# Optimization experiments

Measured on AMD Instinct MI355X. Metric: run time of the kernel, lower is better.

## Reference

```python
import jax, jax.numpy as jnp
import numpy as np

N_QUBITS = 4
DIM = 2 ** N_QUBITS  # 16-dim statevector
KERNEL = 3
STRIDE = 1
PADDING = 1


def _rot_mats(w):
    # PennyLane Rot(phi, theta, omega) = RZ(omega) RY(theta) RZ(phi)
    phi, theta, omega = w[:, 0], w[:, 1], w[:, 2]
    c = jnp.cos(theta / 2)
    s = jnp.sin(theta / 2)
    em = jnp.exp(-0.5j * (phi + omega))
    ep = jnp.exp(0.5j * (phi + omega))
    ed = jnp.exp(0.5j * (phi - omega))
    edm = jnp.exp(-0.5j * (phi - omega))
    row0 = jnp.stack([em * c, -ed * s], axis=-1)
    row1 = jnp.stack([edm * s, ep * c], axis=-1)
    return jnp.stack([row0, row1], axis=-2)  # [n_qubits, 2, 2]


def _apply_1q(state, U, wire):
    # state: [M] + [2]*n, wire axis is 1+wire (wire 0 is most significant)
    s = jnp.moveaxis(state, 1 + wire, -1)
    s = jnp.einsum('...b,ab->...a', s, U)
    return jnp.moveaxis(s, -1, 1 + wire)


def _apply_cnot(state, c, t):
    s = jnp.moveaxis(state, (1 + c, 1 + t), (-2, -1))
    shp = s.shape
    s = s.reshape(shp[:-2] + (4,))[..., jnp.array([0, 1, 3, 2])].reshape(shp)
    return jnp.moveaxis(s, (-2, -1), (1 + c, 1 + t))


def _forward(x, W_pre, b_pre, W_post, b_post, q_weights):
    B, C, L = x.shape
    xp = jnp.pad(x, ((0, 0), (0, 0), (PADDING, PADDING)))
    L_out = (L + 2 * PADDING - KERNEL) // STRIDE + 1
    starts = jnp.arange(L_out) * STRIDE
    # windows: [B, C, L_out, K] -> flatten channel-major like torch reshape
    win = xp[:, :, starts[:, None] + jnp.arange(KERNEL)[None, :]]
    win = win.transpose(0, 2, 1, 3).reshape(B, L_out, C * KERNEL)
    pre = win @ W_pre.T + b_pre  # [B, L_out, n_qubits]
    # AmplitudeEmbedding: pad to 2**n and normalize
    v = jnp.pad(pre, ((0, 0), (0, 0), (0, DIM - N_QUBITS)))
    v = v / jnp.linalg.norm(v, axis=-1, keepdims=True)
    state = v.reshape(B * L_out, *([2] * N_QUBITS)).astype(jnp.complex64)
    U = _rot_mats(q_weights)
    for i in range(N_QUBITS):
        state = _apply_1q(state, U[i], i)
    for i in range(N_QUBITS - 1):
        state = _apply_cnot(state, i, i + 1)
    flat = state.reshape(B * L_out, DIM)
    probs = jnp.real(flat) ** 2 + jnp.imag(flat) ** 2
    # PauliZ expectation per wire: sign of bit i (wire 0 = MSB)
    bits = (jnp.arange(DIM)[None, :] >> (N_QUBITS - 1 - jnp.arange(N_QUBITS)[:, None])) & 1
    z = (1 - 2 * bits).astype(probs.dtype)  # [n_qubits, DIM]
    expz = (probs @ z.T).reshape(B, L_out, N_QUBITS)
    out = expz @ W_post.T + b_post  # [B, L_out, out_channels]
    return out.transpose(0, 2, 1)


def setup_inputs() -> dict:
    key = jax.random.key(0)
    ks = jax.random.split(key, 6)
    B, C, L = 32, 80, 3000
    OUT = 512
    return {
        'x': jax.random.normal(ks[0], (B, C, L), dtype=jnp.float32),
        'W_pre': jax.random.normal(ks[1], (N_QUBITS, C * KERNEL), dtype=jnp.float32) * 0.06,
        'b_pre': jax.random.normal(ks[2], (N_QUBITS,), dtype=jnp.float32) * 0.06,
        'W_post': jax.random.normal(ks[3], (OUT, N_QUBITS), dtype=jnp.float32) * 0.4,
        'b_post': jax.random.normal(ks[4], (OUT,), dtype=jnp.float32) * 0.4,
        'q_weights': jax.random.normal(ks[5], (N_QUBITS, 3), dtype=jnp.float32),
    }


def reference(x, W_pre, b_pre, W_post, b_post, q_weights):
    return _forward(x, W_pre, b_pre, W_post, b_post, q_weights)
```

## Files before the change

kernel.cpp:

```cpp
#include <hip/hip_runtime.h>
#include <math.h>

#define C_IN 80
#define L_IN 3000
#define OUT_C 512
#define NT 512
#define TL 128
#define CPT 20

struct c2f { float x, y; };

__device__ __forceinline__ c2f cmul(c2f a, c2f b) {
    return { a.x*b.x - a.y*b.y, a.x*b.y + a.y*b.x };
}
__device__ __forceinline__ c2f csel(c2f a, c2f b, int bit) {
    c2f r; r.x = bit ? b.x : a.x; r.y = bit ? b.y : a.y; return r;
}
__device__ __forceinline__ float quadform(const float4* __restrict__ A, float4 p) {
    float4 r0 = A[0], r1 = A[1], r2 = A[2], r3 = A[3];
    return p.x*(r0.x*p.x + r0.y*p.y + r0.z*p.z + r0.w*p.w)
         + p.y*(r1.x*p.x + r1.y*p.y + r1.z*p.z + r1.w*p.w)
         + p.z*(r2.x*p.x + r2.y*p.y + r2.z*p.z + r2.w*p.w)
         + p.w*(r3.x*p.x + r3.y*p.y + r3.z*p.z + r3.w*p.w);
}

__global__ __launch_bounds__(NT) void qconv_kernel(
    const float* __restrict__ x,
    const float* __restrict__ W_pre,
    const float* __restrict__ b_pre,
    const float* __restrict__ W_post,
    const float* __restrict__ b_post,
    const float* __restrict__ qw,
    float* __restrict__ out)
{
    __shared__ float4 s_wpre[C_IN*3];
    __shared__ float4 s_post[OUT_C];
    __shared__ float  s_bpost[OUT_C];
    __shared__ float4 s_A[4][4];
    __shared__ float4 s_part[3][TL];
    __shared__ float4 s_e[TL];

    const int t  = threadIdx.x;
    const int b  = blockIdx.y;
    const int l0 = blockIdx.x * TL;

    for (int i = t; i < C_IN*3; i += NT) {
        s_wpre[i] = make_float4(W_pre[0*C_IN*3 + i], W_pre[1*C_IN*3 + i],
                                W_pre[2*C_IN*3 + i], W_pre[3*C_IN*3 + i]);
    }
    if (t < OUT_C) {
        s_post[t]  = *reinterpret_cast<const float4*>(&W_post[t*4]);
        s_bpost[t] = b_post[t];
    }
    __syncthreads();

    if (t < 64) {
        c2f U[4][2][2];
        #pragma unroll
        for (int i = 0; i < 4; ++i) {
            float phi = qw[i*3+0], theta = qw[i*3+1], omega = qw[i*3+2];
            float sh, ch;  sincosf(0.5f*theta, &sh, &ch);
            float s1, c1;  sincosf(0.5f*(phi+omega), &s1, &c1);
            float s2, cv;  sincosf(0.5f*(phi-omega), &s2, &cv);
            U[i][0][0] = {  c1*ch, -s1*ch };
            U[i][0][1] = { -cv*sh, -s2*sh };
            U[i][1][0] = {  cv*sh, -s2*sh };
            U[i][1][1] = {  c1*ch,  s1*ch };
        }
        const int q  = t >> 4;
        const int j  = (t >> 2) & 3;
        const int jp = t & 3;
        const int j2  = (j  >> 1) & 1, j3  = j  & 1;
        const int jp2 = (jp >> 1) & 1, jp3 = jp & 1;
        float s = 0.f;
        #pragma unroll
        for (int k = 0; k < 16; ++k) {
            int m = k ^ ((k >> 1) & 1);
            m ^= ((m >> 2) & 1) << 1;
            m ^= ((m >> 3) & 1) << 2;
            const int m0 = (m >> 3) & 1, m1 = (m >> 2) & 1;
            const int m2 = (m >> 1) & 1, m3 = m & 1;
            c2f w01 = cmul(U[0][m0][0], U[1][m1][0]);
            c2f av = cmul(w01, cmul(csel(U[2][m2][0], U[2][m2][1], j2),
                                    csel(U[3][m3][0], U[3][m3][1], j3)));
            c2f bv = cmul(w01, cmul(csel(U[2][m2][0], U[2][m2][1], jp2),
                                    csel(U[3][m3][0], U[3][m3][1], jp3)));
            float z = 1.f - 2.f * ((k >> (3 - q)) & 1);
            s += z * (av.x*bv.x + av.y*bv.y);
        }
        ((float*)s_A)[t] = s;
    }

    const int i = t & (TL - 1);
    const int h = t >> 7;
    const int l = l0 + i;
    const bool lvalid = (l < L_IN);

    float4 acc = (h == 0) ? make_float4(b_pre[0], b_pre[1], b_pre[2], b_pre[3])
                          : make_float4(0.f, 0.f, 0.f, 0.f);
    if (lvalid) {
        const float* __restrict__ xrow = x + (size_t)b * C_IN * L_IN + (size_t)(h*CPT) * L_IN + l;
        const bool has_m1 = (l >= 1);
        const bool has_p1 = (l + 1 < L_IN);
        #pragma unroll 4
        for (int c = 0; c < CPT; ++c) {
            const float* r = xrow + c * L_IN;
            float xa = has_m1 ? r[-1] : 0.f;
            float xb = r[0];
            float xc = has_p1 ? r[1] : 0.f;
            const int ck = (h*CPT + c) * 3;
            float4 w0 = s_wpre[ck], w1 = s_wpre[ck+1], w2 = s_wpre[ck+2];
            acc.x += w0.x*xa + w1.x*xb + w2.x*xc;
            acc.y += w0.y*xa + w1.y*xb + w2.y*xc;
            acc.z += w0.z*xa + w1.z*xb + w2.z*xc;
            acc.w += w0.w*xa + w1.w*xb + w2.w*xc;
        }
    }
    if (h > 0) s_part[h-1][i] = acc;
    __syncthreads();

    if (t < TL && lvalid) {
        float4 p = acc;
        float4 p1 = s_part[0][t], p2 = s_part[1][t], p3 = s_part[2][t];
        p.x += p1.x + p2.x + p3.x;
        p.y += p1.y + p2.y + p3.y;
        p.z += p1.z + p2.z + p3.z;
        p.w += p1.w + p2.w + p3.w;
        const float inv = 1.f / (p.x*p.x + p.y*p.y + p.z*p.z + p.w*p.w);
        float4 e;
        e.x = quadform(s_A[0], p) * inv;
        e.y = quadform(s_A[1], p) * inv;
        e.z = quadform(s_A[2], p) * inv;
        e.w = quadform(s_A[3], p) * inv;
        s_e[t] = e;
    }
    __syncthreads();

    {
        const int lane = t & 63;
        const int w    = t >> 6;
        const int lc   = l0 + 2*lane;
        const bool v2  = (lc < L_IN);
        const float4 e0 = s_e[2*lane];
        const float4 e1 = s_e[2*lane + 1];
        float* op = out + (size_t)b * OUT_C * L_IN + (size_t)w * L_IN + lc;
        #pragma unroll 8
        for (int k = 0; k < OUT_C/8; ++k) {
            const int o = w + 8*k;
            float4 wv = s_post[o];
            float bb  = s_bpost[o];
            float2 st;
            st.x = wv.x*e0.x + wv.y*e0.y + wv.z*e0.z + wv.w*e0.w + bb;
            st.y = wv.x*e1.x + wv.y*e1.y + wv.z*e1.z + wv.w*e1.w + bb;
            if (v2) *reinterpret_cast<float2*>(op) = st;
            op += (size_t)8 * L_IN;
        }
    }
}

extern "C" void kernel_launch(void* const* d_in, const int* in_sizes, int n_in,
                              void* d_out, int out_size, void* d_ws, size_t ws_size,
                              hipStream_t stream) {
    const float* x      = (const float*)d_in[0];
    const float* W_pre  = (const float*)d_in[1];
    const float* b_pre  = (const float*)d_in[2];
    const float* W_post = (const float*)d_in[3];
    const float* b_post = (const float*)d_in[4];
    const float* qw     = (const float*)d_in[5];
    float* out = (float*)d_out;

    const int B = in_sizes[0] / (C_IN * L_IN);
    dim3 grid((L_IN + TL - 1) / TL, B);
    qconv_kernel<<<grid, NT, 0, stream>>>(x, W_pre, b_pre, W_post, b_post, qw, out);
}
```

Measured before the change: 43.81 us.

## Warp-specialize block so half computes second tile while other half stores first

The block's 128 positions are split into two halves. All 8 warps first compute the pre-projection for the first half, then warps 0-3 emit output rows for it while warps 4-7 compute the second half's projection. Afterwards every warp writes its own 64 output channels for both halves using scalar stores, replacing the earlier float2 stores. The aim is to overlap the input-read and reduction phase with the large output-write phase. It depends on __syncthreads being reached in divergent branches, which is fragile, and the scalar stores may be less efficient than the old float2 ones.

```diff
diff --git a/kernel.cpp b/kernel.cpp
--- a/kernel.cpp
+++ b/kernel.cpp
@@ -6,7 +6,6 @@
 #define OUT_C 512
 #define NT 512
 #define TL 128
-#define CPT 20
 
 struct c2f { float x, y; };
 
@@ -15,13 +14,6 @@
 }
 __device__ __forceinline__ c2f csel(c2f a, c2f b, int bit) {
     c2f r; r.x = bit ? b.x : a.x; r.y = bit ? b.y : a.y; return r;
-}
-__device__ __forceinline__ float quadform(const float4* __restrict__ A, float4 p) {
-    float4 r0 = A[0], r1 = A[1], r2 = A[2], r3 = A[3];
-    return p.x*(r0.x*p.x + r0.y*p.y + r0.z*p.z + r0.w*p.w)
-         + p.y*(r1.x*p.x + r1.y*p.y + r1.z*p.z + r1.w*p.w)
-         + p.z*(r2.x*p.x + r2.y*p.y + r2.z*p.z + r2.w*p.w)
-         + p.w*(r3.x*p.x + r3.y*p.y + r3.z*p.z + r3.w*p.w);
 }
 
 __global__ __launch_bounds__(NT) void qconv_kernel(
@@ -36,23 +28,22 @@
     __shared__ float4 s_wpre[C_IN*3];
     __shared__ float4 s_post[OUT_C];
     __shared__ float  s_bpost[OUT_C];
-    __shared__ float4 s_A[4][4];
-    __shared__ float4 s_part[3][TL];
-    __shared__ float4 s_e[TL];
-
-    const int t  = threadIdx.x;
-    const int b  = blockIdx.y;
-    const int l0 = blockIdx.x * TL;
+    __shared__ float4 s_A[16];
+    __shared__ float4 s_pA[8*64];
+    __shared__ float4 s_pB[4*64];
+
+    const int t    = threadIdx.x;
+    const int w    = t >> 6;
+    const int lane = t & 63;
+    const int b    = blockIdx.y;
+    const int l0   = blockIdx.x * TL;
 
     for (int i = t; i < C_IN*3; i += NT) {
         s_wpre[i] = make_float4(W_pre[0*C_IN*3 + i], W_pre[1*C_IN*3 + i],
                                 W_pre[2*C_IN*3 + i], W_pre[3*C_IN*3 + i]);
     }
-    if (t < OUT_C) {
-        s_post[t]  = *reinterpret_cast<const float4*>(&W_post[t*4]);
-        s_bpost[t] = b_post[t];
-    }
-    __syncthreads();
+    s_post[t]  = *reinterpret_cast<const float4*>(&W_post[t*4]);
+    s_bpost[t] = b_post[t];
 
     if (t < 64) {
         c2f U[4][2][2];
@@ -91,70 +82,130 @@
         ((float*)s_A)[t] = s;
     }
 
-    const int i = t & (TL - 1);
-    const int h = t >> 7;
-    const int l = l0 + i;
-    const bool lvalid = (l < L_IN);
-
-    float4 acc = (h == 0) ? make_float4(b_pre[0], b_pre[1], b_pre[2], b_pre[3])
-                          : make_float4(0.f, 0.f, 0.f, 0.f);
-    if (lvalid) {
-        const float* __restrict__ xrow = x + (size_t)b * C_IN * L_IN + (size_t)(h*CPT) * L_IN + l;
-        const bool has_m1 = (l >= 1);
-        const bool has_p1 = (l + 1 < L_IN);
-        #pragma unroll 4
-        for (int c = 0; c < CPT; ++c) {
-            const float* r = xrow + c * L_IN;
-            float xa = has_m1 ? r[-1] : 0.f;
-            float xb = r[0];
-            float xc = has_p1 ? r[1] : 0.f;
-            const int ck = (h*CPT + c) * 3;
-            float4 w0 = s_wpre[ck], w1 = s_wpre[ck+1], w2 = s_wpre[ck+2];
-            acc.x += w0.x*xa + w1.x*xb + w2.x*xc;
-            acc.y += w0.y*xa + w1.y*xb + w2.y*xc;
-            acc.z += w0.z*xa + w1.z*xb + w2.z*xc;
-            acc.w += w0.w*xa + w1.w*xb + w2.w*xc;
-        }
-    }
-    if (h > 0) s_part[h-1][i] = acc;
+    {
+        const int l = l0 + lane;
+        const bool lv = (l < L_IN);
+        float4 acc = (w == 0) ? make_float4(b_pre[0], b_pre[1], b_pre[2], b_pre[3])
+                              : make_float4(0.f, 0.f, 0.f, 0.f);
+        if (lv) {
+            const float* __restrict__ xr = x + (size_t)b * C_IN * L_IN + (size_t)(w*10) * L_IN + l;
+            const bool hm = (l >= 1), hp = (l + 1 < L_IN);
+            #pragma unroll
+            for (int c = 0; c < 10; ++c) {
+                const float* r = xr + c * L_IN;
+                float xa = hm ? r[-1] : 0.f;
+                float xb = r[0];
+                float xc = hp ? r[1] : 0.f;
+                const int ck = (w*10 + c) * 3;
+                float4 w0 = s_wpre[ck], w1 = s_wpre[ck+1], w2 = s_wpre[ck+2];
+                acc.x += w0.x*xa + w1.x*xb + w2.x*xc;
+                acc.y += w0.y*xa + w1.y*xb + w2.y*xc;
+                acc.z += w0.z*xa + w1.z*xb + w2.z*xc;
+                acc.w += w0.w*xa + w1.w*xb + w2.w*xc;
+            }
+        }
+        s_pA[w*64 + lane] = acc;
+    }
     __syncthreads();
 
-    if (t < TL && lvalid) {
-        float4 p = acc;
-        float4 p1 = s_part[0][t], p2 = s_part[1][t], p3 = s_part[2][t];
-        p.x += p1.x + p2.x + p3.x;
-        p.y += p1.y + p2.y + p3.y;
-        p.z += p1.z + p2.z + p3.z;
-        p.w += p1.w + p2.w + p3.w;
+    auto reduceA = [&]() {
+        float4 p = s_pA[lane];
+        #pragma unroll
+        for (int j = 1; j < 8; ++j) {
+            float4 q2 = s_pA[j*64 + lane];
+            p.x += q2.x; p.y += q2.y; p.z += q2.z; p.w += q2.w;
+        }
+        return p;
+    };
+    auto reduceB = [&]() {
+        float4 p = s_pB[lane];
+        #pragma unroll
+        for (int j = 1; j < 4; ++j) {
+            float4 q2 = s_pB[j*64 + lane];
+            p.x += q2.x; p.y += q2.y; p.z += q2.z; p.w += q2.w;
+        }
+        return p;
+    };
+    auto expz = [&](float4 p) {
         const float inv = 1.f / (p.x*p.x + p.y*p.y + p.z*p.z + p.w*p.w);
         float4 e;
-        e.x = quadform(s_A[0], p) * inv;
-        e.y = quadform(s_A[1], p) * inv;
-        e.z = quadform(s_A[2], p) * inv;
-        e.w = quadform(s_A[3], p) * inv;
-        s_e[t] = e;
-    }
-    __syncthreads();
-
-    {
-        const int lane = t & 63;
-        const int w    = t >> 6;
-        const int lc   = l0 + 2*lane;
-        const bool v2  = (lc < L_IN);
-        const float4 e0 = s_e[2*lane];
-        const float4 e1 = s_e[2*lane + 1];
-        float* op = out + (size_t)b * OUT_C * L_IN + (size_t)w * L_IN + lc;
+        {
+            float4 r0 = s_A[0], r1 = s_A[1], r2 = s_A[2], r3 = s_A[3];
+            e.x = (p.x*(r0.x*p.x + r0.y*p.y + r0.z*p.z + r0.w*p.w)
+                 + p.y*(r1.x*p.x + r1.y*p.y + r1.z*p.z + r1.w*p.w)
+                 + p.z*(r2.x*p.x + r2.y*p.y + r2.z*p.z + r2.w*p.w)
+                 + p.w*(r3.x*p.x + r3.y*p.y + r3.z*p.z + r3.w*p.w)) * inv;
+        }
+        {
+            float4 r0 = s_A[4], r1 = s_A[5], r2 = s_A[6], r3 = s_A[7];
+            e.y = (p.x*(r0.x*p.x + r0.y*p.y + r0.z*p.z + r0.w*p.w)
+                 + p.y*(r1.x*p.x + r1.y*p.y + r1.z*p.z + r1.w*p.w)
+                 + p.z*(r2.x*p.x + r2.y*p.y + r2.z*p.z + r2.w*p.w)
+                 + p.w*(r3.x*p.x + r3.y*p.y + r3.z*p.z + r3.w*p.w)) * inv;
+        }
+        {
+            float4 r0 = s_A[8], r1 = s_A[9], r2 = s_A[10], r3 = s_A[11];
+            e.z = (p.x*(r0.x*p.x + r0.y*p.y + r0.z*p.z + r0.w*p.w)
+                 + p.y*(r1.x*p.x + r1.y*p.y + r1.z*p.z + r1.w*p.w)
+                 + p.z*(r2.x*p.x + r2.y*p.y + r2.z*p.z + r2.w*p.w)
+                 + p.w*(r3.x*p.x + r3.y*p.y + r3.z*p.z + r3.w*p.w)) * inv;
+        }
+        {
+            float4 r0 = s_A[12], r1 = s_A[13], r2 = s_A[14], r3 = s_A[15];
+            e.w = (p.x*(r0.x*p.x + r0.y*p.y + r0.z*p.z + r0.w*p.w)
+                 + p.y*(r1.x*p.x + r1.y*p.y + r1.z*p.z + r1.w*p.w)
+                 + p.z*(r2.x*p.x + r2.y*p.y + r2.z*p.z + r2.w*p.w)
+                 + p.w*(r3.x*p.x + r3.y*p.y + r3.z*p.z + r3.w*p.w)) * inv;
+        }
+        return e;
+    };
+    auto storeRows = [&](float4 e, int obase, int lcol) {
+        const bool lv = (lcol < L_IN);
+        float* op = out + ((size_t)b * OUT_C + obase) * L_IN + lcol;
         #pragma unroll 8
-        for (int k = 0; k < OUT_C/8; ++k) {
-            const int o = w + 8*k;
-            float4 wv = s_post[o];
-            float bb  = s_bpost[o];
-            float2 st;
-            st.x = wv.x*e0.x + wv.y*e0.y + wv.z*e0.z + wv.w*e0.w + bb;
-            st.y = wv.x*e1.x + wv.y*e1.y + wv.z*e1.z + wv.w*e1.w + bb;
-            if (v2) *reinterpret_cast<float2*>(op) = st;
-            op += (size_t)8 * L_IN;
-        }
+        for (int k = 0; k < 64; ++k) {
+            const float4 wv = s_post[obase + k];
+            const float  v = wv.x*e.x + wv.y*e.y + wv.z*e.z + wv.w*e.w + s_bpost[obase + k];
+            if (lv) *op = v;
+            op += L_IN;
+        }
+    };
+
+    if (w < 4) {
+        float4 eH0 = expz(reduceA());
+        storeRows(eH0, w*64, l0 + lane);
+        __syncthreads();
+        float4 eH1 = expz(reduceB());
+        storeRows(eH1, w*64, l0 + 64 + lane);
+    } else {
+        const int sub = w - 4;
+        const int l = l0 + 64 + lane;
+        const bool lv = (l < L_IN);
+        float4 acc = (sub == 0) ? make_float4(b_pre[0], b_pre[1], b_pre[2], b_pre[3])
+                                : make_float4(0.f, 0.f, 0.f, 0.f);
+        if (lv) {
+            const float* __restrict__ xr = x + (size_t)b * C_IN * L_IN + (size_t)(sub*20) * L_IN + l;
+            const bool hm = (l >= 1), hp = (l + 1 < L_IN);
+            #pragma unroll 4
+            for (int c = 0; c < 20; ++c) {
+                const float* r = xr + c * L_IN;
+                float xa = hm ? r[-1] : 0.f;
+                float xb = r[0];
+                float xc = hp ? r[1] : 0.f;
+                const int ck = (sub*20 + c) * 3;
+                float4 w0 = s_wpre[ck], w1 = s_wpre[ck+1], w2 = s_wpre[ck+2];
+                acc.x += w0.x*xa + w1.x*xb + w2.x*xc;
+                acc.y += w0.y*xa + w1.y*xb + w2.y*xc;
+                acc.z += w0.z*xa + w1.z*xb + w2.z*xc;
+                acc.w += w0.w*xa + w1.w*xb + w2.w*xc;
+            }
+        }
+        s_pB[sub*64 + lane] = acc;
+        __syncthreads();
+        float4 eH0 = expz(reduceA());
+        storeRows(eH0, 256 + sub*64, l0 + lane);
+        float4 eH1 = expz(reduceB());
+        storeRows(eH1, 256 + sub*64, l0 + 64 + lane);
     }
 }
 
```

New measurement: 52.76 us. 20.4% more time.

## Widen tile to 192 positions with 768 threads and 16-byte output stores

Applied to the files above, without the earlier changes.

The L-tile grows from 128 to 192 positions and the block from 512 to 768 threads (12 waves), with 4 channel groups of 3 waves each. The output stage now has 48 lanes per wave each write a float4 of four consecutive positions, replacing the earlier float2 stores, to cut store instruction count on the dominant output write. The larger tile divides 3000 into fewer blocks with less tail waste. In exchange, 16 lanes per wave sit idle during the store phase, and occupancy may drop because each block is larger.

```diff
diff --git a/kernel.cpp b/kernel.cpp
--- a/kernel.cpp
+++ b/kernel.cpp
@@ -4,9 +4,12 @@
 #define C_IN 80
 #define L_IN 3000
 #define OUT_C 512
-#define NT 512
-#define TL 128
+#define NT 768
+#define NW 12
+#define TL 192
 #define CPT 20
+
+typedef float floatx4 __attribute__((ext_vector_type(4)));
 
 struct c2f { float x, y; };
 
@@ -36,13 +39,15 @@
     __shared__ float4 s_wpre[C_IN*3];
     __shared__ float4 s_post[OUT_C];
     __shared__ float  s_bpost[OUT_C];
-    __shared__ float4 s_A[4][4];
+    __shared__ float4 s_A[16];
     __shared__ float4 s_part[3][TL];
     __shared__ float4 s_e[TL];
 
-    const int t  = threadIdx.x;
-    const int b  = blockIdx.y;
-    const int l0 = blockIdx.x * TL;
+    const int t    = threadIdx.x;
+    const int w    = t >> 6;
+    const int lane = t & 63;
+    const int b    = blockIdx.y;
+    const int l0   = blockIdx.x * TL;
 
     for (int i = t; i < C_IN*3; i += NT) {
         s_wpre[i] = make_float4(W_pre[0*C_IN*3 + i], W_pre[1*C_IN*3 + i],
@@ -91,23 +96,22 @@
         ((float*)s_A)[t] = s;
     }
 
-    const int i = t & (TL - 1);
-    const int h = t >> 7;
+    const int h = w / 3;
+    const int i = (w % 3) * 64 + lane;
     const int l = l0 + i;
-    const bool lvalid = (l < L_IN);
+    const bool lv = (l < L_IN);
 
     float4 acc = (h == 0) ? make_float4(b_pre[0], b_pre[1], b_pre[2], b_pre[3])
                           : make_float4(0.f, 0.f, 0.f, 0.f);
-    if (lvalid) {
-        const float* __restrict__ xrow = x + (size_t)b * C_IN * L_IN + (size_t)(h*CPT) * L_IN + l;
-        const bool has_m1 = (l >= 1);
-        const bool has_p1 = (l + 1 < L_IN);
-        #pragma unroll 4
+    if (lv) {
+        const float* __restrict__ xr = x + (size_t)b * C_IN * L_IN + (size_t)(h*CPT) * L_IN + l;
+        const bool hm = (l >= 1), hp = (l + 1 < L_IN);
+        #pragma unroll 2
         for (int c = 0; c < CPT; ++c) {
-            const float* r = xrow + c * L_IN;
-            float xa = has_m1 ? r[-1] : 0.f;
+            const float* r = xr + c * L_IN;
+            float xa = hm ? r[-1] : 0.f;
             float xb = r[0];
-            float xc = has_p1 ? r[1] : 0.f;
+            float xc = hp ? r[1] : 0.f;
             const int ck = (h*CPT + c) * 3;
             float4 w0 = s_wpre[ck], w1 = s_wpre[ck+1], w2 = s_wpre[ck+2];
             acc.x += w0.x*xa + w1.x*xb + w2.x*xc;
@@ -119,7 +123,7 @@
     if (h > 0) s_part[h-1][i] = acc;
     __syncthreads();
 
-    if (t < TL && lvalid) {
+    if (t < TL) {
         float4 p = acc;
         float4 p1 = s_part[0][t], p2 = s_part[1][t], p3 = s_part[2][t];
         p.x += p1.x + p2.x + p3.x;
@@ -128,32 +132,35 @@
         p.w += p1.w + p2.w + p3.w;
         const float inv = 1.f / (p.x*p.x + p.y*p.y + p.z*p.z + p.w*p.w);
         float4 e;
-        e.x = quadform(s_A[0], p) * inv;
-        e.y = quadform(s_A[1], p) * inv;
-        e.z = quadform(s_A[2], p) * inv;
-        e.w = quadform(s_A[3], p) * inv;
+        e.x = quadform(&s_A[0],  p) * inv;
+        e.y = quadform(&s_A[4],  p) * inv;
+        e.z = quadform(&s_A[8],  p) * inv;
+        e.w = quadform(&s_A[12], p) * inv;
         s_e[t] = e;
     }
     __syncthreads();
 
-    {
-        const int lane = t & 63;
-        const int w    = t >> 6;
-        const int lc   = l0 + 2*lane;
-        const bool v2  = (lc < L_IN);
-        const float4 e0 = s_e[2*lane];
-        const float4 e1 = s_e[2*lane + 1];
-        float* op = out + (size_t)b * OUT_C * L_IN + (size_t)w * L_IN + lc;
-        #pragma unroll 8
-        for (int k = 0; k < OUT_C/8; ++k) {
-            const int o = w + 8*k;
-            float4 wv = s_post[o];
-            float bb  = s_bpost[o];
-            float2 st;
-            st.x = wv.x*e0.x + wv.y*e0.y + wv.z*e0.z + wv.w*e0.w + bb;
-            st.y = wv.x*e1.x + wv.y*e1.y + wv.z*e1.z + wv.w*e1.w + bb;
-            if (v2) *reinterpret_cast<float2*>(op) = st;
-            op += (size_t)8 * L_IN;
+    if (lane < 48) {
+        const int lq  = l0 + 4*lane;
+        const bool sv = (lq < L_IN);
+        if (sv) {
+            const float4 e0 = s_e[4*lane+0];
+            const float4 e1 = s_e[4*lane+1];
+            const float4 e2 = s_e[4*lane+2];
+            const float4 e3 = s_e[4*lane+3];
+            float* op = out + ((size_t)b * OUT_C + w) * L_IN + lq;
+            #pragma unroll 4
+            for (int o = w; o < OUT_C; o += NW) {
+                const float4 wv = s_post[o];
+                const float  bb = s_bpost[o];
+                floatx4 st;
+                st.x = wv.x*e0.x + wv.y*e0.y + wv.z*e0.z + wv.w*e0.w + bb;
+                st.y = wv.x*e1.x + wv.y*e1.y + wv.z*e1.z + wv.w*e1.w + bb;
+                st.z = wv.x*e2.x + wv.y*e2.y + wv.z*e2.z + wv.w*e2.w + bb;
+                st.w = wv.x*e3.x + wv.y*e3.y + wv.z*e3.z + wv.w*e3.w + bb;
+                *reinterpret_cast<floatx4*>(op) = st;
+                op += (size_t)NW * L_IN;
+            }
         }
     }
 }
```

Result: no change. 44.09 us (+0.6%).
